# Kernel tuning notes

Hardware: AMD Instinct MI355X
Metric: run time of the kernel (lower is better)

## Reference

```python
import jax, jax.numpy as jnp
import numpy as np

N = 100000
E = 3200000
IN_FEAT = 128
OUT_FEAT = 128


def setup_inputs() -> dict:
    key = jax.random.key(0)
    k1, k2, k3, k4, k5, k6 = jax.random.split(key, 6)
    x = jax.random.normal(k1, (N, IN_FEAT), dtype=jnp.float32)
    edge_row = jax.random.randint(k2, (E,), 0, N, dtype=jnp.int32)
    edge_col = jax.random.randint(k3, (E,), 0, N, dtype=jnp.int32)
    edge_weight = jax.random.uniform(k4, (E,), dtype=jnp.float32)
    # nn.Linear(in_feat, out_feat) params
    bound = 1.0 / np.sqrt(IN_FEAT)
    W = jax.random.uniform(k5, (OUT_FEAT, IN_FEAT), dtype=jnp.float32, minval=-bound, maxval=bound)
    b = jax.random.uniform(k6, (OUT_FEAT,), dtype=jnp.float32, minval=-bound, maxval=bound)
    return {"x": x, "edge_row": edge_row, "edge_col": edge_col,
            "edge_weight": edge_weight, "W": W, "b": b, "k": 4}


def _spmm(edge_row, edge_col, edge_weight, x):
    # sparse adj (COO) @ dense x : gather source rows, scale, scatter-add to dest rows
    msgs = edge_weight[:, None] * x[edge_col]          # [E, F]
    return jax.ops.segment_sum(msgs, edge_row, num_segments=N)


def reference(x, edge_row, edge_col, edge_weight, W, b, k):
    for _ in range(k):
        x = _spmm(edge_row, edge_col, edge_weight, x)  # [N, F]
    # nn.Linear: x @ W^T + b
    return x @ W.T + b
```

## Files before the change

### kernel.cpp

```cpp
#include <hip/hip_runtime.h>
#include <hip/hip_fp16.h>


#define F 128
#define CH 2048
#define MAXB 256
#define RB_LOG 9
#define RB (1 << RB_LOG)
#define CAPB 18432

typedef _Float16 half8 __attribute__((ext_vector_type(8)));
typedef float f32x4 __attribute__((ext_vector_type(4)));

__global__ void prep_kernel(const float* __restrict__ W, __half* __restrict__ Wh,
                            int nw, int* __restrict__ bcnt, int nwb) {
  int blk = blockIdx.x;
  if (blk == nwb) {
    int t = threadIdx.x;
    if (t < MAXB) bcnt[t] = 0;
  } else {
    int i = blk * 256 + threadIdx.x;
    if (i < nw) Wh[i] = __float2half(W[i]);
  }
}

__global__ __launch_bounds__(256) void bucket_scatter(
    const int* __restrict__ erow, const int* __restrict__ ecol,
    const float* __restrict__ ew, int* __restrict__ bcnt,
    int2* __restrict__ mid, int e, int nb) {
  __shared__ int  rowv[CH];
  __shared__ int2 cw[CH];
  __shared__ int2 stage[CH];
  __shared__ unsigned short sbid[CH];
  __shared__ int cnt[MAXB], lstart[MAXB], gbase[MAXB], cnt2[MAXB];
  __shared__ int ps[256];
  int tid = threadIdx.x;
  int base = blockIdx.x * CH;
  int tot = e - base; if (tot > CH) tot = CH;
  for (int t = tid; t < nb; t += 256) { cnt[t] = 0; cnt2[t] = 0; }
  __syncthreads();
  for (int j = tid; j < tot; j += 256) {
    int i = base + j;
    int r = erow[i];
    rowv[j] = r;
    cw[j] = make_int2(ecol[i], __float_as_int(ew[i]));
    atomicAdd(&cnt[r >> RB_LOG], 1);
  }
  __syncthreads();
  int v = (tid < nb) ? cnt[tid] : 0;
  ps[tid] = v;
  __syncthreads();
  for (int off = 1; off < 256; off <<= 1) {
    int u = (tid >= off) ? ps[tid - off] : 0;
    __syncthreads();
    ps[tid] += u;
    __syncthreads();
  }
  if (tid < nb) lstart[tid] = ps[tid] - v;
  __syncthreads();
  for (int t = tid; t < nb; t += 256)
    if (cnt[t] > 0) gbase[t] = atomicAdd(&bcnt[t], cnt[t]);
  __syncthreads();
  for (int j = tid; j < tot; j += 256) {
    int r = rowv[j];
    int bb = r >> RB_LOG;
    int k = atomicAdd(&cnt2[bb], 1);
    int p = lstart[bb] + k;
    stage[p] = make_int2(((r & (RB - 1)) << 17) | cw[j].x, cw[j].y);
    sbid[p] = (unsigned short)bb;
  }
  __syncthreads();
  for (int j = tid; j < tot; j += 256) {
    int bb = sbid[j];
    mid[(size_t)bb * CAPB + gbase[bb] + (j - lstart[bb])] = stage[j];
  }
}

__global__ __launch_bounds__(256) void csr_sort(
    const int2* __restrict__ mid, const int* __restrict__ bcnt,
    int* __restrict__ rptr, int2* __restrict__ edges, int n, int nb) {
  __shared__ int rcnt[RB];
  __shared__ int rofs[RB];
  __shared__ int psum[256];
  __shared__ int2 st[CAPB];
  int b = blockIdx.x, tid = threadIdx.x;
  int r0 = b << RB_LOG;
  int r1 = r0 + RB; if (r1 > n) r1 = n;
  int nr = r1 - r0;
  int cnt = bcnt[b];
  const int2* src = mid + (size_t)b * CAPB;

  psum[tid] = (tid < b && tid < nb) ? bcnt[tid] : 0;
  __syncthreads();
  for (int off = 128; off > 0; off >>= 1) {
    if (tid < off) psum[tid] += psum[tid + off];
    __syncthreads();
  }
  int bas = psum[0];
  __syncthreads();

  for (int r = tid; r < RB; r += 256) rcnt[r] = 0;
  __syncthreads();
  for (int i = tid; i < cnt; i += 256)
    atomicAdd(&rcnt[((unsigned)src[i].x) >> 17], 1);
  __syncthreads();
  int s2 = rcnt[2 * tid] + rcnt[2 * tid + 1];
  psum[tid] = s2;
  __syncthreads();
  for (int off = 1; off < 256; off <<= 1) {
    int u = (tid >= off) ? psum[tid - off] : 0;
    __syncthreads();
    psum[tid] += u;
    __syncthreads();
  }
  int ex = (tid > 0) ? psum[tid - 1] : 0;
  rofs[2 * tid]     = ex;
  rofs[2 * tid + 1] = ex + rcnt[2 * tid];
  __syncthreads();
  for (int r = tid; r < nr; r += 256) rptr[r0 + r] = bas + rofs[r];
  if (b == nb - 1 && tid == 0) rptr[n] = bas + cnt;
  for (int i = tid; i < cnt; i += 256) {
    int2 ed = src[i];
    int rl  = ((unsigned)ed.x) >> 17;
    int col = ed.x & 0x1FFFF;
    int p = atomicAdd(&rofs[rl], 1);
    st[p] = make_int2(col << 8, ed.y);
  }
  __syncthreads();
  for (int i = tid; i < cnt; i += 256) edges[bas + i] = st[i];
}

__global__ __launch_bounds__(256, 8) void spmm_kernel(
    const int* __restrict__ rptr, const int2* __restrict__ edges,
    const __half* __restrict__ xin, __half* __restrict__ xout, int n) {
  int lane = threadIdx.x & 63;
  int hid = lane >> 5;
  int fl  = lane & 31;
  int row = (blockIdx.x << 2) + (threadIdx.x >> 6);
  if (row >= n) return;
  int s = rptr[row], e = rptr[row + 1];
  float4 acc = make_float4(0.f, 0.f, 0.f, 0.f);
  float4 ac2 = make_float4(0.f, 0.f, 0.f, 0.f);
  const char* xb = (const char*)xin;

#define GATHER_FMA(ED, A)                                                     \
  {                                                                           \
    float w = __int_as_float((ED).y);                                         \
    short4 hv = *(const short4*)(xb + (size_t)(unsigned)(ED).x + (fl << 3));  \
    union { short2 s2; __half2 h2; } u0, u1;                                  \
    u0.s2 = make_short2(hv.x, hv.y);                                          \
    u1.s2 = make_short2(hv.z, hv.w);                                          \
    float2 f0 = __half22float2(u0.h2);                                        \
    float2 f1 = __half22float2(u1.h2);                                        \
    A.x = fmaf(w, f0.x, A.x); A.y = fmaf(w, f0.y, A.y);                       \
    A.z = fmaf(w, f1.x, A.z); A.w = fmaf(w, f1.y, A.w);                       \
  }

  int i = s;
  for (; i + 7 < e; i += 8) {
    int2 e0 = edges[i + hid];
    int2 e1 = edges[i + 2 + hid];
    int2 e2 = edges[i + 4 + hid];
    int2 e3 = edges[i + 6 + hid];
    GATHER_FMA(e0, acc); GATHER_FMA(e1, ac2);
    GATHER_FMA(e2, acc); GATHER_FMA(e3, ac2);
  }
  for (; i + 1 < e; i += 2) {
    int2 e0 = edges[i + hid];
    GATHER_FMA(e0, acc);
  }
  if (i < e && hid == 0) {
    int2 e0 = edges[i];
    GATHER_FMA(e0, acc);
  }
#undef GATHER_FMA

  acc.x += ac2.x; acc.y += ac2.y; acc.z += ac2.z; acc.w += ac2.w;
  acc.x += __shfl_xor(acc.x, 32, 64);
  acc.y += __shfl_xor(acc.y, 32, 64);
  acc.z += __shfl_xor(acc.z, 32, 64);
  acc.w += __shfl_xor(acc.w, 32, 64);
  if (hid == 0) {
    union { short4 s4; __half2 h2[2]; } o;
    o.h2[0] = __float22half2_rn(make_float2(acc.x, acc.y));
    o.h2[1] = __float22half2_rn(make_float2(acc.z, acc.w));
    *(short4*)((char*)xout + ((size_t)row << 8) + (fl << 3)) = o.s4;
  }
}

__global__ void f32_to_f16(const float2* __restrict__ in, __half2* __restrict__ out, int n2) {
  int i = blockIdx.x * blockDim.x + threadIdx.x;
  if (i < n2) out[i] = __float22half2_rn(in[i]);
}

__global__ __launch_bounds__(256) void linear_mfma(
    const __half* __restrict__ xin, const __half* __restrict__ Wh,
    const float* __restrict__ b, float* __restrict__ out, int n) {
  int lane = threadIdx.x & 63;
  int wv   = threadIdx.x >> 6;
  int rbase = blockIdx.x * 64 + wv * 16;
  if (rbase >= n) return;
  int arow = rbase + (lane & 15);
  if (arow >= n) arow = n - 1;
  int koff = (lane >> 4) * 8;

  half8 a0 = *(const half8*)(xin + (size_t)arow * F + 0  + koff);
  half8 a1 = *(const half8*)(xin + (size_t)arow * F + 32 + koff);
  half8 a2 = *(const half8*)(xin + (size_t)arow * F + 64 + koff);
  half8 a3 = *(const half8*)(xin + (size_t)arow * F + 96 + koff);

  int drow0 = rbase + (lane >> 4) * 4;
  int dcol  = lane & 15;
#pragma unroll
  for (int jt = 0; jt < 8; ++jt) {
    const __half* wrow = Wh + (size_t)(jt * 16 + (lane & 15)) * F + koff;
    half8 b0 = *(const half8*)(wrow + 0);
    half8 b1 = *(const half8*)(wrow + 32);
    half8 b2 = *(const half8*)(wrow + 64);
    half8 b3 = *(const half8*)(wrow + 96);
    f32x4 acc = {0.f, 0.f, 0.f, 0.f};
    acc = __builtin_amdgcn_mfma_f32_16x16x32_f16(a0, b0, acc, 0, 0, 0);
    acc = __builtin_amdgcn_mfma_f32_16x16x32_f16(a1, b1, acc, 0, 0, 0);
    acc = __builtin_amdgcn_mfma_f32_16x16x32_f16(a2, b2, acc, 0, 0, 0);
    acc = __builtin_amdgcn_mfma_f32_16x16x32_f16(a3, b3, acc, 0, 0, 0);
    float bias = b[jt * 16 + dcol];
#pragma unroll
    for (int m = 0; m < 4; ++m) {
      int r = drow0 + m;
      if (r < n) out[(size_t)r * F + jt * 16 + dcol] = acc[m] + bias;
    }
  }
}

extern "C" void kernel_launch(void* const* d_in, const int* in_sizes, int n_in,
                              void* d_out, int out_size, void* d_ws, size_t ws_size,
                              hipStream_t stream) {
  const float* x    = (const float*)d_in[0];
  const int*   erow = (const int*)d_in[1];
  const int*   ecol = (const int*)d_in[2];
  const float* ew   = (const float*)d_in[3];
  const float* W    = (const float*)d_in[4];
  const float* b    = (const float*)d_in[5];
  float* out = (float*)d_out;

  const int N = in_sizes[0] / F;
  const int E = in_sizes[1];

  char* ws = (char*)d_ws;
  size_t off = 0;
  int2*  edges  = (int2*)(ws + off);   off += (size_t)E * 8;
  int*   rptr   = (int*)(ws + off);    off += (size_t)(N + 1) * 4;
  int*   bcnt   = (int*)(ws + off);    off += MAXB * 4;
  off = (off + 255) & ~(size_t)255;
  __half* Wh    = (__half*)(ws + off); off += (size_t)F * F * 2;
  off = (off + 255) & ~(size_t)255;
  __half2* bufA = (__half2*)(ws + off);
  __half2* bufB = (__half2*)(ws + off + (size_t)N * F * 2);
  int2*    mid  = (int2*)bufA;

  const int BK = 256;
  int nb = (N + RB - 1) >> RB_LOG;
  int nwb = (F * F + BK - 1) / BK;

  prep_kernel<<<nwb + 1, BK, 0, stream>>>(W, Wh, F * F, bcnt, nwb);
  bucket_scatter<<<(E + CH - 1) / CH, 256, 0, stream>>>(erow, ecol, ew, bcnt, mid, E, nb);
  csr_sort<<<nb, 256, 0, stream>>>(mid, bcnt, rptr, edges, N, nb);

  int n2 = N * (F / 2);
  f32_to_f16<<<(n2 + BK - 1) / BK, BK, 0, stream>>>((const float2*)x, bufB, n2);
  int spmm_grid = (N + 3) / 4;
  spmm_kernel<<<spmm_grid, 256, 0, stream>>>(rptr, edges, (const __half*)bufB, (__half*)bufA, N);
  spmm_kernel<<<spmm_grid, 256, 0, stream>>>(rptr, edges, (const __half*)bufA, (__half*)bufB, N);
  spmm_kernel<<<spmm_grid, 256, 0, stream>>>(rptr, edges, (const __half*)bufB, (__half*)bufA, N);
  spmm_kernel<<<spmm_grid, 256, 0, stream>>>(rptr, edges, (const __half*)bufA, (__half*)bufB, N);

  linear_mfma<<<(N + 63) / 64, 256, 0, stream>>>((const __half*)bufB, Wh, b, out, N);
}
```

Measured before the change: 589.3 us.

## Split features into two 64-wide slices so SpMM gathers fit in cache

The 128-wide fp16 feature matrix is split into two 64-column slices, and the four propagation steps run separately on each slice. Each SpMM gather then reads a 12.8 MB table instead of 25.6 MB, so it can stay resident in the last-level cache. Edge data is stored as separate int column and fp16 weight arrays to shrink the edge stream. The cost is twice as many SpMM launches, rereading the edge list eight times instead of four, narrower 4-byte gathers per lane, and weights rounded to fp16.

```diff
diff --git a/kernel.cpp b/kernel.cpp
--- a/kernel.cpp
+++ b/kernel.cpp
@@ -3,6 +3,7 @@
 
 
 #define F 128
+#define SLICE_H 64
 #define CH 2048
 #define MAXB 256
 #define RB_LOG 9
@@ -78,7 +79,8 @@
 
 __global__ __launch_bounds__(256) void csr_sort(
     const int2* __restrict__ mid, const int* __restrict__ bcnt,
-    int* __restrict__ rptr, int2* __restrict__ edges, int n, int nb) {
+    int* __restrict__ rptr, int* __restrict__ ecols, __half* __restrict__ ewh,
+    int n, int nb) {
   __shared__ int rcnt[RB];
   __shared__ int rofs[RB];
   __shared__ int psum[256];
@@ -124,14 +126,19 @@
     int rl  = ((unsigned)ed.x) >> 17;
     int col = ed.x & 0x1FFFF;
     int p = atomicAdd(&rofs[rl], 1);
-    st[p] = make_int2(col << 8, ed.y);
-  }
-  __syncthreads();
-  for (int i = tid; i < cnt; i += 256) edges[bas + i] = st[i];
-}
-
-__global__ __launch_bounds__(256, 8) void spmm_kernel(
-    const int* __restrict__ rptr, const int2* __restrict__ edges,
+    st[p] = make_int2(col, ed.y);
+  }
+  __syncthreads();
+  for (int i = tid; i < cnt; i += 256) {
+    int2 ed = st[i];
+    ecols[bas + i] = ed.x;
+    ewh[bas + i]   = __float2half(__int_as_float(ed.y));
+  }
+}
+
+__global__ __launch_bounds__(256) void spmm_slice(
+    const int* __restrict__ rptr, const int* __restrict__ ecols,
+    const __half* __restrict__ ewh,
     const __half* __restrict__ xin, __half* __restrict__ xout, int n) {
   int lane = threadIdx.x & 63;
   int hid = lane >> 5;
@@ -139,63 +146,70 @@
   int row = (blockIdx.x << 2) + (threadIdx.x >> 6);
   if (row >= n) return;
   int s = rptr[row], e = rptr[row + 1];
-  float4 acc = make_float4(0.f, 0.f, 0.f, 0.f);
-  float4 ac2 = make_float4(0.f, 0.f, 0.f, 0.f);
+  float2 a0 = make_float2(0.f, 0.f), a1 = make_float2(0.f, 0.f);
   const char* xb = (const char*)xin;
 
-#define GATHER_FMA(ED, A)                                                     \
+#define GFMA(COL, WH, A)                                                      \
   {                                                                           \
-    float w = __int_as_float((ED).y);                                         \
-    short4 hv = *(const short4*)(xb + (size_t)(unsigned)(ED).x + (fl << 3));  \
-    union { short2 s2; __half2 h2; } u0, u1;                                  \
-    u0.s2 = make_short2(hv.x, hv.y);                                          \
-    u1.s2 = make_short2(hv.z, hv.w);                                          \
-    float2 f0 = __half22float2(u0.h2);                                        \
-    float2 f1 = __half22float2(u1.h2);                                        \
-    A.x = fmaf(w, f0.x, A.x); A.y = fmaf(w, f0.y, A.y);                       \
-    A.z = fmaf(w, f1.x, A.z); A.w = fmaf(w, f1.y, A.w);                       \
+    float w = __half2float(WH);                                               \
+    union { int i; __half2 h2; } u;                                           \
+    u.i = *(const int*)(xb + ((size_t)(unsigned)(COL) << 7) + (fl << 2));     \
+    float2 f = __half22float2(u.h2);                                          \
+    A.x = fmaf(w, f.x, A.x); A.y = fmaf(w, f.y, A.y);                         \
   }
 
   int i = s;
+  if ((i & 1) && i < e) {
+    if (hid == 0) GFMA(ecols[i], ewh[i], a0);
+    ++i;
+  }
+  union { uint u; __half2 h2; } wp0, wp1, wp2, wp3;
   for (; i + 7 < e; i += 8) {
-    int2 e0 = edges[i + hid];
-    int2 e1 = edges[i + 2 + hid];
-    int2 e2 = edges[i + 4 + hid];
-    int2 e3 = edges[i + 6 + hid];
-    GATHER_FMA(e0, acc); GATHER_FMA(e1, ac2);
-    GATHER_FMA(e2, acc); GATHER_FMA(e3, ac2);
+    int2 c0 = *(const int2*)&ecols[i];
+    int2 c1 = *(const int2*)&ecols[i + 2];
+    int2 c2 = *(const int2*)&ecols[i + 4];
+    int2 c3 = *(const int2*)&ecols[i + 6];
+    wp0.u = *(const uint*)&ewh[i];
+    wp1.u = *(const uint*)&ewh[i + 2];
+    wp2.u = *(const uint*)&ewh[i + 4];
+    wp3.u = *(const uint*)&ewh[i + 6];
+    int k0 = hid ? c0.y : c0.x;  __half w0 = hid ? wp0.h2.y : wp0.h2.x;
+    int k1 = hid ? c1.y : c1.x;  __half w1 = hid ? wp1.h2.y : wp1.h2.x;
+    int k2 = hid ? c2.y : c2.x;  __half w2 = hid ? wp2.h2.y : wp2.h2.x;
+    int k3 = hid ? c3.y : c3.x;  __half w3 = hid ? wp3.h2.y : wp3.h2.x;
+    GFMA(k0, w0, a0); GFMA(k1, w1, a1);
+    GFMA(k2, w2, a0); GFMA(k3, w3, a1);
   }
   for (; i + 1 < e; i += 2) {
-    int2 e0 = edges[i + hid];
-    GATHER_FMA(e0, acc);
-  }
-  if (i < e && hid == 0) {
-    int2 e0 = edges[i];
-    GATHER_FMA(e0, acc);
-  }
-#undef GATHER_FMA
-
-  acc.x += ac2.x; acc.y += ac2.y; acc.z += ac2.z; acc.w += ac2.w;
-  acc.x += __shfl_xor(acc.x, 32, 64);
-  acc.y += __shfl_xor(acc.y, 32, 64);
-  acc.z += __shfl_xor(acc.z, 32, 64);
-  acc.w += __shfl_xor(acc.w, 32, 64);
+    int2 c0 = *(const int2*)&ecols[i];
+    wp0.u = *(const uint*)&ewh[i];
+    int k0 = hid ? c0.y : c0.x;  __half w0 = hid ? wp0.h2.y : wp0.h2.x;
+    GFMA(k0, w0, a0);
+  }
+  if (i < e && hid == 0) GFMA(ecols[i], ewh[i], a0);
+#undef GFMA
+
+  a0.x += a1.x; a0.y += a1.y;
+  a0.x += __shfl_xor(a0.x, 32, 64);
+  a0.y += __shfl_xor(a0.y, 32, 64);
   if (hid == 0) {
-    union { short4 s4; __half2 h2[2]; } o;
-    o.h2[0] = __float22half2_rn(make_float2(acc.x, acc.y));
-    o.h2[1] = __float22half2_rn(make_float2(acc.z, acc.w));
-    *(short4*)((char*)xout + ((size_t)row << 8) + (fl << 3)) = o.s4;
-  }
-}
-
-__global__ void f32_to_f16(const float2* __restrict__ in, __half2* __restrict__ out, int n2) {
-  int i = blockIdx.x * blockDim.x + threadIdx.x;
-  if (i < n2) out[i] = __float22half2_rn(in[i]);
+    __half2 o = __float22half2_rn(a0);
+    *(__half2*)((char*)xout + ((size_t)row << 7) + (fl << 2)) = o;
+  }
+}
+
+__global__ void f32_to_f16_slice(const float2* __restrict__ in,
+                                 __half2* __restrict__ dst, int n, int soff) {
+  int t = blockIdx.x * blockDim.x + threadIdx.x;
+  if (t >= n * 32) return;
+  int row = t >> 5, d = t & 31;
+  dst[row * 32 + d] = __float22half2_rn(in[(size_t)row * 64 + soff + d]);
 }
 
 __global__ __launch_bounds__(256) void linear_mfma(
-    const __half* __restrict__ xin, const __half* __restrict__ Wh,
-    const float* __restrict__ b, float* __restrict__ out, int n) {
+    const __half* __restrict__ s0, const __half* __restrict__ s1,
+    const __half* __restrict__ Wh, const float* __restrict__ b,
+    float* __restrict__ out, int n) {
   int lane = threadIdx.x & 63;
   int wv   = threadIdx.x >> 6;
   int rbase = blockIdx.x * 64 + wv * 16;
@@ -204,10 +218,10 @@
   if (arow >= n) arow = n - 1;
   int koff = (lane >> 4) * 8;
 
-  half8 a0 = *(const half8*)(xin + (size_t)arow * F + 0  + koff);
-  half8 a1 = *(const half8*)(xin + (size_t)arow * F + 32 + koff);
-  half8 a2 = *(const half8*)(xin + (size_t)arow * F + 64 + koff);
-  half8 a3 = *(const half8*)(xin + (size_t)arow * F + 96 + koff);
+  half8 a0 = *(const half8*)(s0 + (size_t)arow * SLICE_H + 0  + koff);
+  half8 a1 = *(const half8*)(s0 + (size_t)arow * SLICE_H + 32 + koff);
+  half8 a2 = *(const half8*)(s1 + (size_t)arow * SLICE_H + 0  + koff);
+  half8 a3 = *(const half8*)(s1 + (size_t)arow * SLICE_H + 32 + koff);
 
   int drow0 = rbase + (lane >> 4) * 4;
   int dcol  = lane & 15;
@@ -248,15 +262,20 @@
 
   char* ws = (char*)d_ws;
   size_t off = 0;
-  int2*  edges  = (int2*)(ws + off);   off += (size_t)E * 8;
+  int*    ecols = (int*)(ws + off);    off += (size_t)E * 4;
+  __half* ewh   = (__half*)(ws + off); off += (size_t)E * 2;
+  off = (off + 255) & ~(size_t)255;
   int*   rptr   = (int*)(ws + off);    off += (size_t)(N + 1) * 4;
   int*   bcnt   = (int*)(ws + off);    off += MAXB * 4;
   off = (off + 255) & ~(size_t)255;
   __half* Wh    = (__half*)(ws + off); off += (size_t)F * F * 2;
   off = (off + 255) & ~(size_t)255;
-  __half2* bufA = (__half2*)(ws + off);
-  __half2* bufB = (__half2*)(ws + off + (size_t)N * F * 2);
-  int2*    mid  = (int2*)bufA;
+  size_t sbytes = (size_t)N * SLICE_H * 2;
+  __half* s0A = (__half*)(ws + off);
+  __half* s0B = (__half*)(ws + off + sbytes);
+  __half* s1A = (__half*)(ws + off + 2 * sbytes);
+  __half* s1B = (__half*)(ws + off + 3 * sbytes);
+  int2*   mid = (int2*)s0A;
 
   const int BK = 256;
   int nb = (N + RB - 1) >> RB_LOG;
@@ -264,15 +283,20 @@
 
   prep_kernel<<<nwb + 1, BK, 0, stream>>>(W, Wh, F * F, bcnt, nwb);
   bucket_scatter<<<(E + CH - 1) / CH, 256, 0, stream>>>(erow, ecol, ew, bcnt, mid, E, nb);
-  csr_sort<<<nb, 256, 0, stream>>>(mid, bcnt, rptr, edges, N, nb);
-
-  int n2 = N * (F / 2);
-  f32_to_f16<<<(n2 + BK - 1) / BK, BK, 0, stream>>>((const float2*)x, bufB, n2);
+  csr_sort<<<nb, 256, 0, stream>>>(mid, bcnt, rptr, ecols, ewh, N, nb);
+
+  int cgrid = (N * 32 + BK - 1) / BK;
+  f32_to_f16_slice<<<cgrid, BK, 0, stream>>>((const float2*)x, (__half2*)s0A, N, 0);
+  f32_to_f16_slice<<<cgrid, BK, 0, stream>>>((const float2*)x, (__half2*)s1A, N, 32);
   int spmm_grid = (N + 3) / 4;
-  spmm_kernel<<<spmm_grid, 256, 0, stream>>>(rptr, edges, (const __half*)bufB, (__half*)bufA, N);
-  spmm_kernel<<<spmm_grid, 256, 0, stream>>>(rptr, edges, (const __half*)bufA, (__half*)bufB, N);
-  spmm_kernel<<<spmm_grid, 256, 0, stream>>>(rptr, edges, (const __half*)bufB, (__half*)bufA, N);
-  spmm_kernel<<<spmm_grid, 256, 0, stream>>>(rptr, edges, (const __half*)bufA, (__half*)bufB, N);
-
-  linear_mfma<<<(N + 63) / 64, 256, 0, stream>>>((const __half*)bufB, Wh, b, out, N);
-}
+  spmm_slice<<<spmm_grid, 256, 0, stream>>>(rptr, ecols, ewh, s0A, s0B, N);
+  spmm_slice<<<spmm_grid, 256, 0, stream>>>(rptr, ecols, ewh, s0B, s0A, N);
+  spmm_slice<<<spmm_grid, 256, 0, stream>>>(rptr, ecols, ewh, s0A, s0B, N);
+  spmm_slice<<<spmm_grid, 256, 0, stream>>>(rptr, ecols, ewh, s0B, s0A, N);
+  spmm_slice<<<spmm_grid, 256, 0, stream>>>(rptr, ecols, ewh, s1A, s1B, N);
+  spmm_slice<<<spmm_grid, 256, 0, stream>>>(rptr, ecols, ewh, s1B, s1A, N);
+  spmm_slice<<<spmm_grid, 256, 0, stream>>>(rptr, ecols, ewh, s1A, s1B, N);
+  spmm_slice<<<spmm_grid, 256, 0, stream>>>(rptr, ecols, ewh, s1B, s1A, N);
+
+  linear_mfma<<<(N + 63) / 64, 256, 0, stream>>>(s0A, s1A, Wh, b, out, N);
+}
```

Result: slower. 759.3 us (+28.8%).

## Split edges into column and fp16 weight arrays, gather 16B per lane over four edges

Applied to the files above, without the earlier changes.

The packed int2 edge array is replaced by a separate int column array and an fp16 weight array, shrinking edge metadata from 8 to 6 bytes per edge. The SpMM kernel now has 16 lanes cover a 256-byte row with 16-byte loads and processes four edges in parallel per wave, then reduces across the four quarter-waves with two shuffles. The launch-bounds occupancy hint is dropped. Converting weights to fp16 adds extra rounding error, and the wider per-lane accumulators raise register pressure.

```diff
diff --git a/kernel.cpp b/kernel.cpp
--- a/kernel.cpp
+++ b/kernel.cpp
@@ -78,7 +78,8 @@
 
 __global__ __launch_bounds__(256) void csr_sort(
     const int2* __restrict__ mid, const int* __restrict__ bcnt,
-    int* __restrict__ rptr, int2* __restrict__ edges, int n, int nb) {
+    int* __restrict__ rptr, int* __restrict__ ecols, __half* __restrict__ ewh,
+    int n, int nb) {
   __shared__ int rcnt[RB];
   __shared__ int rofs[RB];
   __shared__ int psum[256];
@@ -124,67 +125,80 @@
     int rl  = ((unsigned)ed.x) >> 17;
     int col = ed.x & 0x1FFFF;
     int p = atomicAdd(&rofs[rl], 1);
-    st[p] = make_int2(col << 8, ed.y);
-  }
-  __syncthreads();
-  for (int i = tid; i < cnt; i += 256) edges[bas + i] = st[i];
-}
-
-__global__ __launch_bounds__(256, 8) void spmm_kernel(
-    const int* __restrict__ rptr, const int2* __restrict__ edges,
+    st[p] = make_int2(col, ed.y);
+  }
+  __syncthreads();
+  for (int i = tid; i < cnt; i += 256) {
+    int2 ed = st[i];
+    ecols[bas + i] = ed.x;
+    ewh[bas + i]   = __float2half(__int_as_float(ed.y));
+  }
+}
+
+__global__ __launch_bounds__(256) void spmm_kernel(
+    const int* __restrict__ rptr, const int* __restrict__ ecols,
+    const __half* __restrict__ ewh,
     const __half* __restrict__ xin, __half* __restrict__ xout, int n) {
   int lane = threadIdx.x & 63;
-  int hid = lane >> 5;
-  int fl  = lane & 31;
+  int q  = lane >> 4;
+  int fl = lane & 15;
   int row = (blockIdx.x << 2) + (threadIdx.x >> 6);
   if (row >= n) return;
   int s = rptr[row], e = rptr[row + 1];
-  float4 acc = make_float4(0.f, 0.f, 0.f, 0.f);
-  float4 ac2 = make_float4(0.f, 0.f, 0.f, 0.f);
+  float a00 = 0.f, a01 = 0.f, a02 = 0.f, a03 = 0.f;
+  float a04 = 0.f, a05 = 0.f, a06 = 0.f, a07 = 0.f;
+  float b00 = 0.f, b01 = 0.f, b02 = 0.f, b03 = 0.f;
+  float b04 = 0.f, b05 = 0.f, b06 = 0.f, b07 = 0.f;
   const char* xb = (const char*)xin;
-
-#define GATHER_FMA(ED, A)                                                     \
+  union V { int4 i4; __half2 h2[4]; };
+
+#define UNPACK_FMA(U, W, P)                                                   \
   {                                                                           \
-    float w = __int_as_float((ED).y);                                         \
-    short4 hv = *(const short4*)(xb + (size_t)(unsigned)(ED).x + (fl << 3));  \
-    union { short2 s2; __half2 h2; } u0, u1;                                  \
-    u0.s2 = make_short2(hv.x, hv.y);                                          \
-    u1.s2 = make_short2(hv.z, hv.w);                                          \
-    float2 f0 = __half22float2(u0.h2);                                        \
-    float2 f1 = __half22float2(u1.h2);                                        \
-    A.x = fmaf(w, f0.x, A.x); A.y = fmaf(w, f0.y, A.y);                       \
-    A.z = fmaf(w, f1.x, A.z); A.w = fmaf(w, f1.y, A.w);                       \
+    float2 f0 = __half22float2((U).h2[0]);                                    \
+    float2 f1 = __half22float2((U).h2[1]);                                    \
+    float2 f2 = __half22float2((U).h2[2]);                                    \
+    float2 f3 = __half22float2((U).h2[3]);                                    \
+    P##0 = fmaf((W), f0.x, P##0); P##1 = fmaf((W), f0.y, P##1);               \
+    P##2 = fmaf((W), f1.x, P##2); P##3 = fmaf((W), f1.y, P##3);               \
+    P##4 = fmaf((W), f2.x, P##4); P##5 = fmaf((W), f2.y, P##5);               \
+    P##6 = fmaf((W), f3.x, P##6); P##7 = fmaf((W), f3.y, P##7);               \
   }
 
   int i = s;
   for (; i + 7 < e; i += 8) {
-    int2 e0 = edges[i + hid];
-    int2 e1 = edges[i + 2 + hid];
-    int2 e2 = edges[i + 4 + hid];
-    int2 e3 = edges[i + 6 + hid];
-    GATHER_FMA(e0, acc); GATHER_FMA(e1, ac2);
-    GATHER_FMA(e2, acc); GATHER_FMA(e3, ac2);
-  }
-  for (; i + 1 < e; i += 2) {
-    int2 e0 = edges[i + hid];
-    GATHER_FMA(e0, acc);
-  }
-  if (i < e && hid == 0) {
-    int2 e0 = edges[i];
-    GATHER_FMA(e0, acc);
-  }
-#undef GATHER_FMA
-
-  acc.x += ac2.x; acc.y += ac2.y; acc.z += ac2.z; acc.w += ac2.w;
-  acc.x += __shfl_xor(acc.x, 32, 64);
-  acc.y += __shfl_xor(acc.y, 32, 64);
-  acc.z += __shfl_xor(acc.z, 32, 64);
-  acc.w += __shfl_xor(acc.w, 32, 64);
-  if (hid == 0) {
-    union { short4 s4; __half2 h2[2]; } o;
-    o.h2[0] = __float22half2_rn(make_float2(acc.x, acc.y));
-    o.h2[1] = __float22half2_rn(make_float2(acc.z, acc.w));
-    *(short4*)((char*)xout + ((size_t)row << 8) + (fl << 3)) = o.s4;
+    int   c0 = ecols[i + q];
+    int   c1 = ecols[i + 4 + q];
+    float w0 = __half2float(ewh[i + q]);
+    float w1 = __half2float(ewh[i + 4 + q]);
+    V v0, v1;
+    v0.i4 = *(const int4*)(xb + ((size_t)(unsigned)c0 << 8) + (fl << 4));
+    v1.i4 = *(const int4*)(xb + ((size_t)(unsigned)c1 << 8) + (fl << 4));
+    UNPACK_FMA(v0, w0, a0);
+    UNPACK_FMA(v1, w1, b0);
+  }
+  for (; i < e; i += 4) {
+    int idx = i + q;
+    bool ok = idx < e;
+    int   c = ecols[ok ? idx : e - 1];
+    float w = ok ? __half2float(ewh[idx]) : 0.f;
+    V v;
+    v.i4 = *(const int4*)(xb + ((size_t)(unsigned)c << 8) + (fl << 4));
+    UNPACK_FMA(v, w, a0);
+  }
+#undef UNPACK_FMA
+
+  a00 += b00; a01 += b01; a02 += b02; a03 += b03;
+  a04 += b04; a05 += b05; a06 += b06; a07 += b07;
+#define RED(X) X += __shfl_xor(X, 16, 64); X += __shfl_xor(X, 32, 64);
+  RED(a00) RED(a01) RED(a02) RED(a03) RED(a04) RED(a05) RED(a06) RED(a07)
+#undef RED
+  if (q == 0) {
+    union V o;
+    o.h2[0] = __float22half2_rn(make_float2(a00, a01));
+    o.h2[1] = __float22half2_rn(make_float2(a02, a03));
+    o.h2[2] = __float22half2_rn(make_float2(a04, a05));
+    o.h2[3] = __float22half2_rn(make_float2(a06, a07));
+    *(int4*)((char*)xout + ((size_t)row << 8) + (fl << 4)) = o.i4;
   }
 }
 
@@ -248,15 +262,17 @@
 
   char* ws = (char*)d_ws;
   size_t off = 0;
-  int2*  edges  = (int2*)(ws + off);   off += (size_t)E * 8;
+  int*    ecols = (int*)(ws + off);    off += (size_t)E * 4;
+  __half* ewh   = (__half*)(ws + off); off += (size_t)E * 2;
+  off = (off + 255) & ~(size_t)255;
   int*   rptr   = (int*)(ws + off);    off += (size_t)(N + 1) * 4;
   int*   bcnt   = (int*)(ws + off);    off += MAXB * 4;
   off = (off + 255) & ~(size_t)255;
   __half* Wh    = (__half*)(ws + off); off += (size_t)F * F * 2;
   off = (off + 255) & ~(size_t)255;
-  __half2* bufA = (__half2*)(ws + off);
-  __half2* bufB = (__half2*)(ws + off + (size_t)N * F * 2);
-  int2*    mid  = (int2*)bufA;
+  __half* bufA = (__half*)(ws + off);
+  __half* bufB = (__half*)(ws + off + (size_t)N * F * 2);
+  int2*   mid  = (int2*)bufA;
 
   const int BK = 256;
   int nb = (N + RB - 1) >> RB_LOG;
@@ -264,15 +280,15 @@
 
   prep_kernel<<<nwb + 1, BK, 0, stream>>>(W, Wh, F * F, bcnt, nwb);
   bucket_scatter<<<(E + CH - 1) / CH, 256, 0, stream>>>(erow, ecol, ew, bcnt, mid, E, nb);
-  csr_sort<<<nb, 256, 0, stream>>>(mid, bcnt, rptr, edges, N, nb);
+  csr_sort<<<nb, 256, 0, stream>>>(mid, bcnt, rptr, ecols, ewh, N, nb);
 
   int n2 = N * (F / 2);
-  f32_to_f16<<<(n2 + BK - 1) / BK, BK, 0, stream>>>((const float2*)x, bufB, n2);
+  f32_to_f16<<<(n2 + BK - 1) / BK, BK, 0, stream>>>((const float2*)x, (__half2*)bufB, n2);
   int spmm_grid = (N + 3) / 4;
-  spmm_kernel<<<spmm_grid, 256, 0, stream>>>(rptr, edges, (const __half*)bufB, (__half*)bufA, N);
-  spmm_kernel<<<spmm_grid, 256, 0, stream>>>(rptr, edges, (const __half*)bufA, (__half*)bufB, N);
-  spmm_kernel<<<spmm_grid, 256, 0, stream>>>(rptr, edges, (const __half*)bufB, (__half*)bufA, N);
-  spmm_kernel<<<spmm_grid, 256, 0, stream>>>(rptr, edges, (const __half*)bufA, (__half*)bufB, N);
-
-  linear_mfma<<<(N + 63) / 64, 256, 0, stream>>>((const __half*)bufB, Wh, b, out, N);
-}
+  spmm_kernel<<<spmm_grid, 256, 0, stream>>>(rptr, ecols, ewh, bufB, bufA, N);
+  spmm_kernel<<<spmm_grid, 256, 0, stream>>>(rptr, ecols, ewh, bufA, bufB, N);
+  spmm_kernel<<<spmm_grid, 256, 0, stream>>>(rptr, ecols, ewh, bufB, bufA, N);
+  spmm_kernel<<<spmm_grid, 256, 0, stream>>>(rptr, ecols, ewh, bufA, bufB, N);
+
+  linear_mfma<<<(N + 63) / 64, 256, 0, stream>>>(bufB, Wh, b, out, N);
+}
```

Measured after the change: 561.5 us. -4.7%, faster.
